# Optimization experiments

Hardware: AMD Instinct MI355X
Metric: run time of the kernel (lower is better)

Reference implementation:

```python
import jax, jax.numpy as jnp
import numpy as np

B, S, C, D, V, T = 64, 200, 32, 256, 10000, 1000


def _gru(x, Wih, Whh, bih, bhh):
    # x: [B,S,D]; PyTorch GRU, gate order (r, z, n)
    xp = jnp.einsum('bsd,gd->bsg', x, Wih) + bih  # [B,S,3D] input projections precomputed

    def step(h, xt):
        hp = h @ Whh.T + bhh
        xr, xz, xn = jnp.split(xt, 3, axis=-1)
        hr, hz, hn = jnp.split(hp, 3, axis=-1)
        r = jax.nn.sigmoid(xr + hr)
        z = jax.nn.sigmoid(xz + hz)
        n = jnp.tanh(xn + r * hn)
        h = (1.0 - z) * n + z * h
        return h, h

    h0 = jnp.zeros((x.shape[0], Whh.shape[1]), x.dtype)
    _, hs = jax.lax.scan(step, h0, jnp.swapaxes(xp, 0, 1))
    return jnp.swapaxes(hs, 0, 1)


def _pool(rnn, wl_W, wl_b, out_W, out_b):
    w = jnp.einsum('bsd,od->bso', rnn, wl_W) + wl_b      # [B,S,1]
    att = jax.nn.softmax(w[..., 0], axis=1)               # softmax over seq
    feat = jnp.sum(rnn * att[:, :, None], axis=1)         # [B,D]
    return feat @ out_W.T + out_b                          # [B,2]


def setup_inputs() -> dict:
    key = jax.random.key(0)
    ks = jax.random.split(key, 24)

    def n(i, shape, s=0.05):
        return jax.random.normal(ks[i], shape, dtype=jnp.float32) * s

    inp = {}
    inp['input_seqs'] = jax.random.randint(ks[0], (B, S, C), 0, V)
    inp['masks'] = jnp.ones((B, S), jnp.float32)
    inp['lengths'] = jax.random.randint(ks[1], (B,), 1, S)
    inp['seq_time_step'] = jax.random.uniform(ks[2], (B, S), dtype=jnp.float32)
    inp['code_masks'] = jnp.ones((B, S, C), jnp.float32)
    inp['diffusion_t'] = jax.random.randint(ks[3], (B,), 0, T)
    # parameters
    inp['emb_table'] = n(4, (V + 1, D)).at[V].set(0.0)  # padding_idx row zeroed
    inp['gru_Wih'] = n(5, (3 * D, D))
    inp['gru_Whh'] = n(6, (3 * D, D))
    inp['gru_bih'] = n(7, (3 * D,))
    inp['gru_bhh'] = n(8, (3 * D,))
    inp['whk_W'] = n(9, (D, D))
    inp['whk_b'] = n(10, (D,))
    inp['w1_W'] = n(11, (64, 2 * D))
    inp['w1_b'] = n(12, (64,))
    inp['w2_W'] = n(13, (2, 64))
    inp['w2_b'] = n(14, (2,))
    inp['wl_W'] = n(15, (1, D))
    inp['wl_b'] = n(16, (1,))
    inp['out_W'] = n(17, (2, D))
    inp['out_b'] = n(18, (2,))
    inp['betas'] = jnp.linspace(1e-4, 2e-2, T).astype(jnp.float32)  # linear beta schedule
    inp['W_diff'] = n(19, (S, S))      # surrogate for UNet denoiser (see notes)
    inp['time_scale'] = n(20, (T,), 1.0)
    inp['normal_noise'] = jax.random.normal(ks[21], (B, S, D), dtype=jnp.float32)
    return inp


def reference(input_seqs, masks, lengths, seq_time_step, code_masks, diffusion_t,
              emb_table, gru_Wih, gru_Whh, gru_bih, gru_bhh,
              whk_W, whk_b, w1_W, w1_b, w2_W, w2_b, wl_W, wl_b, out_W, out_b,
              betas, W_diff, time_scale, normal_noise):
    # embedding sum over codes per visit (dropout is identity at eval)
    x = jnp.take(emb_table, input_seqs, axis=0).sum(axis=2)  # [B,S,D]
    rnn = _gru(x, gru_Wih, gru_Whh, gru_bih, gru_bhh)

    # per-timestep attention-gated blend. In the original, e_k is ALWAYS x[:,0:1]
    # and each step depends only on precomputed rnn[:, i-1], so the sequential
    # Python loop vectorizes exactly over the time axis.
    e_k = x[:, 0:1, :]                                              # [B,1,D]
    w_prev = jnp.einsum('bsd,ed->bse', rnn[:, :-1, :], whk_W) + whk_b  # [B,S-1,D]
    cat = jnp.concatenate([jnp.broadcast_to(e_k, w_prev.shape), w_prev], axis=-1)
    h = jnp.tanh(jnp.einsum('bse,fe->bsf', cat, w1_W) + w1_b)
    attn = jax.nn.softmax(jnp.einsum('bsf,gf->bsg', h, w2_W) + w2_b, axis=-1)  # [B,S-1,2]
    blended = e_k * attn[..., 0:1] + w_prev * attn[..., 1:2]
    aligned = jnp.concatenate([x[:, 0:1, :], blended], axis=1)      # [B,S,D]

    # diffusion forward noising
    alpha = jnp.cumprod(1.0 - betas)[diffusion_t][:, None, None]    # [B,1,1]
    x_noisy = aligned * jnp.sqrt(alpha) + normal_noise * jnp.sqrt(1.0 - alpha)
    # surrogate denoiser over channel(=seq) axis, timestep-conditioned
    predicted_noise = jnp.einsum('cs,bsd->bcd', W_diff, x_noisy) * time_scale[diffusion_t][:, None, None]

    gen_x = aligned + (normal_noise - predicted_noise)
    gen_rnn = _gru(gen_x, gru_Wih, gru_Whh, gru_bih, gru_bhh)

    pred = _pool(rnn, wl_W, wl_b, out_W, out_b)
    gen_pred = _pool(gen_rnn, wl_W, wl_b, out_W, out_b)
    return pred, gen_pred, predicted_noise, normal_noise
```

## Files before the change

kernel.cpp:

```cpp
#include <hip/hip_runtime.h>
#include <math.h>

constexpr int Bn = 64, Sn = 200, Cn = 32, Dn = 256, Vn = 10000, Tn = 1000;
constexpr int G3 = 3 * Dn;
constexpr int KP = 224;

typedef __fp16 h2_t __attribute__((ext_vector_type(2)));
typedef short bf16x8 __attribute__((ext_vector_type(8)));
typedef float f32x4 __attribute__((ext_vector_type(4)));

static __device__ __forceinline__ h2_t as_h2(uint v) {
  union { uint u; h2_t h; } c; c.u = v; return c.h;
}
static __device__ __forceinline__ uint as_u32(h2_t h) {
  union { h2_t h; uint u; } c; c.h = h; return c.u;
}
static __device__ __forceinline__ ushort f2bf(float f) {
  uint u = __float_as_uint(f);
  u += 0x7FFFu + ((u >> 16) & 1u);
  return (ushort)(u >> 16);
}

__global__ __launch_bounds__(256) void k_w2f16(const float* __restrict__ w,
    uint* __restrict__ o, int npairs) {
  int i = blockIdx.x * 256 + threadIdx.x;
  if (i < npairs) {
    h2_t pk = __builtin_amdgcn_cvt_pkrtz(w[2 * i], w[2 * i + 1]);
    o[i] = as_u32(pk);
  }
}

__global__ __launch_bounds__(256) void k_w2bf(const float* __restrict__ w,
    ushort* __restrict__ o, int n) {
  int i = blockIdx.x * 256 + threadIdx.x;
  if (i < n) o[i] = f2bf(w[i]);
}

__global__ __launch_bounds__(256) void k_wd2bf(const float* __restrict__ w,
    ushort* __restrict__ o) {
  int i = blockIdx.x * 256 + threadIdx.x;
  if (i < Sn * KP) {
    int r = i / KP, c = i % KP;
    o[i] = (c < Sn) ? f2bf(w[r * Sn + c]) : (ushort)0;
  }
}

__global__ __launch_bounds__(256) void k_embed_sum(const int* __restrict__ seqs,
    const float* __restrict__ emb, float* __restrict__ x, ushort* __restrict__ xbf) {
  const int bs = blockIdx.x;
  const int d = threadIdx.x;
  const int* row = seqs + (size_t)bs * Cn;
  float acc = 0.f;
#pragma unroll
  for (int c = 0; c < Cn; ++c) acc += emb[(size_t)row[c] * Dn + d];
  x[(size_t)bs * Dn + d] = acc;
  xbf[(size_t)bs * Dn + d] = f2bf(acc);
}

__global__ __launch_bounds__(256) void k_gemm_bf16(const ushort* __restrict__ A,
    const ushort* __restrict__ Bm, const float* __restrict__ bias,
    float* __restrict__ C, int M, int N) {
  __shared__ ushort As[64 * 40];
  __shared__ ushort Bs[64 * 40];
  const int tid = threadIdx.x;
  const int m0 = blockIdx.x * 64, n0 = blockIdx.y * 64;
  const int wave = tid >> 6, lane = tid & 63;
  const int wr = wave >> 1, wc = wave & 1;
  const int lrow = tid >> 2, lseg = (tid & 3) * 8;
  const int r16 = lane & 15, kg = lane >> 4;
  f32x4 acc[2][2] = {};
  for (int k0 = 0; k0 < 256; k0 += 32) {
    *(uint4*)&As[lrow * 40 + lseg] =
        *(const uint4*)&A[(size_t)(m0 + lrow) * 256 + k0 + lseg];
    *(uint4*)&Bs[lrow * 40 + lseg] =
        *(const uint4*)&Bm[(size_t)(n0 + lrow) * 256 + k0 + lseg];
    __syncthreads();
    bf16x8 a0 = *(const bf16x8*)&As[(wr * 32 + r16) * 40 + kg * 8];
    bf16x8 a1 = *(const bf16x8*)&As[(wr * 32 + 16 + r16) * 40 + kg * 8];
    bf16x8 b0 = *(const bf16x8*)&Bs[(wc * 32 + r16) * 40 + kg * 8];
    bf16x8 b1 = *(const bf16x8*)&Bs[(wc * 32 + 16 + r16) * 40 + kg * 8];
    acc[0][0] = __builtin_amdgcn_mfma_f32_16x16x32_bf16(a0, b0, acc[0][0], 0, 0, 0);
    acc[0][1] = __builtin_amdgcn_mfma_f32_16x16x32_bf16(a0, b1, acc[0][1], 0, 0, 0);
    acc[1][0] = __builtin_amdgcn_mfma_f32_16x16x32_bf16(a1, b0, acc[1][0], 0, 0, 0);
    acc[1][1] = __builtin_amdgcn_mfma_f32_16x16x32_bf16(a1, b1, acc[1][1], 0, 0, 0);
    __syncthreads();
  }
#pragma unroll
  for (int mi = 0; mi < 2; ++mi)
#pragma unroll
    for (int ni = 0; ni < 2; ++ni)
#pragma unroll
      for (int r = 0; r < 4; ++r) {
        int gr = m0 + wr * 32 + mi * 16 + kg * 4 + r;
        int gc = n0 + wc * 32 + ni * 16 + r16;
        C[(size_t)gr * N + gc] = acc[mi][ni][r] + bias[gc];
      }
}

__global__ __launch_bounds__(768, 3) void k_gru_g(const float* __restrict__ xp,
    const uint* __restrict__ Wh, const float* __restrict__ bhh,
    float* __restrict__ out, ushort* __restrict__ out_bf) {
  const int b = blockIdx.x;
  const int tid = threadIdx.x;
  const int g = tid >> 8;
  const int d = tid & 255;
  __shared__ uint h2s[2][128];
  __shared__ float red[768];

  uint w_[128];
#pragma unroll
  for (int i = 0; i < 128; i += 4) {
    uint4 v = *reinterpret_cast<const uint4*>(Wh + (size_t)(g * 256 + d) * 128 + i);
    w_[i] = v.x; w_[i + 1] = v.y; w_[i + 2] = v.z; w_[i + 3] = v.w;
  }
  const float* xpb = xp + (size_t)b * Sn * G3;
  const float bias = bhh[g * 256 + d];
  float xv = (g == 2) ? 0.f : xpb[g * 256 + d];
  float xnv = (g == 0) ? xpb[512 + d] : 0.f;
  float h_old = 0.f;
  if (tid < 128) h2s[0][tid] = 0u;
  __syncthreads();

  for (int t = 0; t < Sn; ++t) {
    const int cur = t & 1;
    float a0 = 0.f, a1 = 0.f;
#pragma unroll
    for (int c = 0; c < 8; ++c) {
      uint4 v0 = *reinterpret_cast<const uint4*>(&h2s[cur][8 * c]);
      uint4 v1 = *reinterpret_cast<const uint4*>(&h2s[cur][8 * c + 4]);
      uint hh[8] = {v0.x, v0.y, v0.z, v0.w, v1.x, v1.y, v1.z, v1.w};
#pragma unroll
      for (int i = 0; i < 8; ++i)
        a0 = __builtin_amdgcn_fdot2(as_h2(w_[8 * c + i]), as_h2(hh[i]), a0, false);
    }
#pragma unroll
    for (int c = 8; c < 16; ++c) {
      uint4 v0 = *reinterpret_cast<const uint4*>(&h2s[cur][8 * c]);
      uint4 v1 = *reinterpret_cast<const uint4*>(&h2s[cur][8 * c + 4]);
      uint hh[8] = {v0.x, v0.y, v0.z, v0.w, v1.x, v1.y, v1.z, v1.w};
#pragma unroll
      for (int i = 0; i < 8; ++i)
        a1 = __builtin_amdgcn_fdot2(as_h2(w_[8 * c + i]), as_h2(hh[i]), a1, false);
    }
    red[tid] = a0 + a1 + xv + bias;
    float xnv_c = xnv;
    if (t + 1 < Sn) {
      const float* xr = xpb + (size_t)(t + 1) * G3;
      if (g != 2) xv = xr[g * 256 + d];
      if (g == 0) xnv = xr[512 + d];
    }
    __syncthreads();
    if (g == 0) {
      float rv = 1.f / (1.f + __expf(-red[d]));
      float zv = 1.f / (1.f + __expf(-red[256 + d]));
      float nv = tanhf(xnv_c + rv * red[512 + d]);
      float h = (1.f - zv) * nv + zv * h_old;
      h_old = h;
      const size_t oi = ((size_t)b * Sn + t) * Dn + d;
      out[oi] = h;
      if (out_bf) out_bf[oi] = f2bf(h);
      float hp2 = __shfl_xor(h, 1);
      if ((d & 1) == 0) h2s[cur ^ 1][d >> 1] = as_u32(__builtin_amdgcn_cvt_pkrtz(h, hp2));
    }
    __syncthreads();
  }
}

__global__ __launch_bounds__(256) void k_attn_par(const float* __restrict__ x,
    const float* __restrict__ wprev, const float* __restrict__ w1W,
    const float* __restrict__ w1b, const float* __restrict__ w2W,
    const float* __restrict__ w2b, float* __restrict__ aligned) {
  extern __shared__ float sm[];
  float* w1s = sm;
  float* ek  = w1s + 64 * 513;
  float* wp  = ek + 256;
  float* eks = wp + 256;
  float* t1  = eks + 64;
  float* a01 = t1 + 64;
  const int b = blockIdx.x, cy = blockIdx.y, tid = threadIdx.x;
  for (int idx = tid; idx < 64 * 512; idx += 256) {
    int f = idx >> 9, c = idx & 511;
    w1s[f * 513 + c] = w1W[idx];
  }
  ek[tid] = x[(size_t)b * Sn * Dn + tid];
  __syncthreads();
  const int f = tid >> 2, kq = tid & 3;
  {
    float p = 0.f;
    const float* wr = w1s + f * 513;
#pragma unroll 8
    for (int j = 0; j < 64; ++j) {
      int k = 64 * kq + ((j + 16 * kq) & 63);
      p += ek[k] * wr[k];
    }
    p += __shfl_xor(p, 1);
    p += __shfl_xor(p, 2);
    if (kq == 0) eks[f] = p + w1b[f];
  }
  if (cy == 0) aligned[(size_t)b * Sn * Dn + tid] = ek[tid];
  __syncthreads();
  const int s0 = 1 + cy * 29;
  const int s1 = (s0 + 29 < Sn) ? s0 + 29 : Sn;
  for (int s = s0; s < s1; ++s) {
    wp[tid] = wprev[((size_t)b * Sn + (s - 1)) * Dn + tid];
    __syncthreads();
    float p = 0.f;
    const float* wr = w1s + f * 513 + 256;
#pragma unroll 8
    for (int j = 0; j < 64; ++j) {
      int k = 64 * kq + ((j + 16 * kq) & 63);
      p += wp[k] * wr[k];
    }
    p += __shfl_xor(p, 1);
    p += __shfl_xor(p, 2);
    if (kq == 0) t1[f] = tanhf(eks[f] + p);
    __syncthreads();
    if (tid == 0) {
      float l0 = w2b[0], l1 = w2b[1];
#pragma unroll
      for (int j = 0; j < 64; ++j) { l0 += t1[j] * w2W[j]; l1 += t1[j] * w2W[64 + j]; }
      float m = fmaxf(l0, l1);
      float e0 = __expf(l0 - m), e1 = __expf(l1 - m);
      float inv = 1.f / (e0 + e1);
      a01[0] = e0 * inv; a01[1] = e1 * inv;
    }
    __syncthreads();
    aligned[((size_t)b * Sn + s) * Dn + tid] = ek[tid] * a01[0] + wp[tid] * a01[1];
    __syncthreads();
  }
}

__global__ __launch_bounds__(256) void k_cumsetup(const float* __restrict__ betas,
    const int* __restrict__ difft, const float* __restrict__ tscale,
    float* __restrict__ sa, float* __restrict__ sb, float* __restrict__ tsv) {
  __shared__ float bl[Tn];
  const int tid = threadIdx.x;
  for (int i = tid; i < Tn; i += 256) bl[i] = betas[i];
  __syncthreads();
  if (tid == 0) {
    float p = 1.f;
    for (int t = 0; t < Tn; ++t) { p *= (1.f - bl[t]); bl[t] = p; }
  }
  __syncthreads();
  if (tid < Bn) {
    int tb = difft[tid];
    float a = bl[tb];
    sa[tid] = sqrtf(a);
    sb[tid] = sqrtf(1.f - a);
    tsv[tid] = tscale[tb];
  }
}

__global__ __launch_bounds__(256) void k_noisy_t(const float* __restrict__ aligned,
    const float* __restrict__ noise, const float* __restrict__ sa,
    const float* __restrict__ sb, ushort* __restrict__ xnT) {
  __shared__ float T[256][33];
  const int b = blockIdx.x, sy = blockIdx.y;
  const int tid = threadIdx.x;
  const float A = sa[b], Bc = sb[b];
#pragma unroll 4
  for (int i = 0; i < 32; ++i) {
    int s = 32 * sy + i;
    float v = 0.f;
    if (s < Sn) {
      size_t idx = ((size_t)b * Sn + s) * Dn + tid;
      v = aligned[idx] * A + noise[idx] * Bc;
    }
    T[tid][i] = v;
  }
  __syncthreads();
  const int sl = tid & 31, dq = tid >> 5;
#pragma unroll 4
  for (int dd = 0; dd < 32; ++dd) {
    int d = dq * 32 + dd;
    xnT[((size_t)b * Dn + d) * KP + 32 * sy + sl] = f2bf(T[d][sl]);
  }
}

__global__ __launch_bounds__(256) void k_diff_mfma(const ushort* __restrict__ Wd_bf,
    const ushort* __restrict__ xnT, const float* __restrict__ tsv,
    const float* __restrict__ aligned, const float* __restrict__ noise,
    float* __restrict__ pn, ushort* __restrict__ genx_bf) {
  __shared__ ushort As[64 * 40];
  __shared__ ushort Bs[64 * 40];
  const int bz = blockIdx.z;
  const int tid = threadIdx.x;
  const int m0 = blockIdx.x * 64, n0 = blockIdx.y * 64;
  const int wave = tid >> 6, lane = tid & 63;
  const int wr = wave >> 1, wc = wave & 1;
  const int lrow = tid >> 2, lseg = (tid & 3) * 8;
  const int r16 = lane & 15, kg = lane >> 4;
  const ushort* Bb = xnT + (size_t)bz * Dn * KP;
  f32x4 acc[2][2] = {};
  for (int k0 = 0; k0 < KP; k0 += 32) {
    uint4 av = {0u, 0u, 0u, 0u};
    if (m0 + lrow < Sn)
      av = *(const uint4*)&Wd_bf[(size_t)(m0 + lrow) * KP + k0 + lseg];
    *(uint4*)&As[lrow * 40 + lseg] = av;
    *(uint4*)&Bs[lrow * 40 + lseg] =
        *(const uint4*)&Bb[(size_t)(n0 + lrow) * KP + k0 + lseg];
    __syncthreads();
    bf16x8 a0 = *(const bf16x8*)&As[(wr * 32 + r16) * 40 + kg * 8];
    bf16x8 a1 = *(const bf16x8*)&As[(wr * 32 + 16 + r16) * 40 + kg * 8];
    bf16x8 b0 = *(const bf16x8*)&Bs[(wc * 32 + r16) * 40 + kg * 8];
    bf16x8 b1 = *(const bf16x8*)&Bs[(wc * 32 + 16 + r16) * 40 + kg * 8];
    acc[0][0] = __builtin_amdgcn_mfma_f32_16x16x32_bf16(a0, b0, acc[0][0], 0, 0, 0);
    acc[0][1] = __builtin_amdgcn_mfma_f32_16x16x32_bf16(a0, b1, acc[0][1], 0, 0, 0);
    acc[1][0] = __builtin_amdgcn_mfma_f32_16x16x32_bf16(a1, b0, acc[1][0], 0, 0, 0);
    acc[1][1] = __builtin_amdgcn_mfma_f32_16x16x32_bf16(a1, b1, acc[1][1], 0, 0, 0);
    __syncthreads();
  }
  const float ts = tsv[bz];
#pragma unroll
  for (int mi = 0; mi < 2; ++mi)
#pragma unroll
    for (int ni = 0; ni < 2; ++ni)
#pragma unroll
      for (int r = 0; r < 4; ++r) {
        int gr = m0 + wr * 32 + mi * 16 + kg * 4 + r;
        int gc = n0 + wc * 32 + ni * 16 + r16;
        if (gr < Sn) {
          size_t idx = ((size_t)bz * Sn + gr) * Dn + gc;
          float val = acc[mi][ni][r] * ts;
          pn[idx] = val;
          genx_bf[idx] = f2bf(aligned[idx] + noise[idx] - val);
        }
      }
}

__global__ __launch_bounds__(256) void k_pool(const float* __restrict__ rnn,
    const float* __restrict__ wlW, const float* __restrict__ wlb,
    const float* __restrict__ outW, const float* __restrict__ outb,
    float* __restrict__ out2) {
  const int b = blockIdx.x, tid = threadIdx.x;
  __shared__ float wl[Dn], att[256], red[256], feat[Dn];
  wl[tid] = wlW[tid];
  __syncthreads();
  float wv = -1e30f;
  if (tid < Sn) {
    const float* r = rnn + ((size_t)b * Sn + tid) * Dn;
    float a = wlb[0];
    for (int k = 0; k < Dn; ++k) a += r[k] * wl[k];
    wv = a;
  }
  red[tid] = wv;
  __syncthreads();
  for (int off = 128; off > 0; off >>= 1) {
    if (tid < off) red[tid] = fmaxf(red[tid], red[tid + off]);
    __syncthreads();
  }
  const float m = red[0];
  __syncthreads();
  float e = (tid < Sn) ? __expf(wv - m) : 0.f;
  red[tid] = e;
  __syncthreads();
  for (int off = 128; off > 0; off >>= 1) {
    if (tid < off) red[tid] += red[tid + off];
    __syncthreads();
  }
  const float inv = 1.f / red[0];
  att[tid] = e * inv;
  __syncthreads();
  const float* rb = rnn + (size_t)b * Sn * Dn;
  float a = 0.f;
  for (int s = 0; s < Sn; ++s) a += rb[(size_t)s * Dn + tid] * att[s];
  feat[tid] = a;
  __syncthreads();
  if (tid < 2) {
    float acc = outb[tid];
    for (int k = 0; k < Dn; ++k) acc += feat[k] * outW[tid * Dn + k];
    out2[b * 2 + tid] = acc;
  }
}

extern "C" void kernel_launch(void* const* d_in, const int* in_sizes, int n_in,
                              void* d_out, int out_size, void* d_ws, size_t ws_size,
                              hipStream_t stream) {
  const int*   seqs   = (const int*)  d_in[0];
  const int*   difft  = (const int*)  d_in[5];
  const float* emb    = (const float*)d_in[6];
  const float* Wih    = (const float*)d_in[7];
  const float* Whh    = (const float*)d_in[8];
  const float* bih    = (const float*)d_in[9];
  const float* bhh    = (const float*)d_in[10];
  const float* whkW   = (const float*)d_in[11];
  const float* whkb   = (const float*)d_in[12];
  const float* w1W    = (const float*)d_in[13];
  const float* w1b    = (const float*)d_in[14];
  const float* w2W    = (const float*)d_in[15];
  const float* w2b    = (const float*)d_in[16];
  const float* wlW    = (const float*)d_in[17];
  const float* wlb    = (const float*)d_in[18];
  const float* outW   = (const float*)d_in[19];
  const float* outb   = (const float*)d_in[20];
  const float* betas  = (const float*)d_in[21];
  const float* Wd     = (const float*)d_in[22];
  const float* tscale = (const float*)d_in[23];
  const float* noise  = (const float*)d_in[24];

  float* ws = (float*)d_ws;
  const size_t NX  = (size_t)Bn * Sn * Dn;
  const size_t NXP = (size_t)Bn * Sn * G3;
  float* x       = ws;
  float* xp      = ws + NX;
  ushort* xnT    = (ushort*)xp;
  float* aligned = xp + NX;
  float* rnn     = ws + NX + NXP;
  float* wprev   = ws + 2 * NX + NXP;
  ushort* x_bf   = (ushort*)wprev;
  ushort* genx_bf= (ushort*)wprev;
  float* sa      = ws + 3 * NX + NXP;
  float* sb      = sa + 64;
  float* tsv     = sb + 64;
  uint*  Wf16    = (uint*)(tsv + 64);
  ushort* rnn_bf = (ushort*)(Wf16 + 98304);
  ushort* Wih_bf = rnn_bf + NX;
  ushort* whk_bf = Wih_bf + 196608;
  ushort* Wd_bf  = whk_bf + 65536;

  float* out       = (float*)d_out;
  float* pred      = out;
  float* gpred     = out + 128;
  float* pn        = out + 256;
  float* out_noise = out + 256 + NX;

  const int ATTN_SMEM = (64 * 513 + 256 + 256 + 64 + 64 + 2) * 4;

  k_w2f16<<<dim3(384), dim3(256), 0, stream>>>(Whh, Wf16, 98304);
  k_w2bf<<<dim3(768), dim3(256), 0, stream>>>(Wih, Wih_bf, 196608);
  k_w2bf<<<dim3(256), dim3(256), 0, stream>>>(whkW, whk_bf, 65536);
  k_wd2bf<<<dim3(175), dim3(256), 0, stream>>>(Wd, Wd_bf);
  k_embed_sum<<<dim3(Bn * Sn), dim3(Dn), 0, stream>>>(seqs, emb, x, x_bf);
  k_gemm_bf16<<<dim3(200, 12), dim3(256), 0, stream>>>(x_bf, Wih_bf, bih, xp, Bn * Sn, G3);
  k_gru_g<<<dim3(Bn), dim3(768), 0, stream>>>(xp, Wf16, bhh, rnn, rnn_bf);
  k_gemm_bf16<<<dim3(200, 4), dim3(256), 0, stream>>>(rnn_bf, whk_bf, whkb, wprev, Bn * Sn, Dn);
  k_attn_par<<<dim3(Bn, 7), dim3(256), ATTN_SMEM, stream>>>(x, wprev, w1W, w1b, w2W, w2b, aligned);
  k_cumsetup<<<dim3(1), dim3(256), 0, stream>>>(betas, difft, tscale, sa, sb, tsv);
  k_noisy_t<<<dim3(Bn, 7), dim3(256), 0, stream>>>(aligned, noise, sa, sb, xnT);
  k_diff_mfma<<<dim3(4, 4, Bn), dim3(256), 0, stream>>>(Wd_bf, xnT, tsv, aligned, noise, pn, genx_bf);
  k_gemm_bf16<<<dim3(200, 12), dim3(256), 0, stream>>>(genx_bf, Wih_bf, bih, xp, Bn * Sn, G3);
  k_gru_g<<<dim3(Bn), dim3(768), 0, stream>>>(xp, Wf16, bhh, wprev, (ushort*)nullptr);
  k_pool<<<dim3(Bn), dim3(256), 0, stream>>>(rnn, wlW, wlb, outW, outb, pred);
  k_pool<<<dim3(Bn), dim3(256), 0, stream>>>(wprev, wlW, wlb, outW, outb, gpred);
  (void)hipMemcpyAsync(out_noise, noise, NX * sizeof(float), hipMemcpyDeviceToDevice, stream);
}
```

Baseline: 1.018 ms.

## Restructure GRU matvec thread mapping with swizzled weights and bf16-only outputs

The GRU recurrent kernel now has each group of 4 threads split the K dimension of 4 gate rows. Weights are pre-permuted with a bank-conflict-avoiding swizzle, so each thread reads one 16-byte LDS chunk per j and reuses it across 4 rows, with shuffles combining partial sums. This targets LDS traffic and bank conflicts on the serial recurrence path. The GRU also stops writing fp32 hidden states, and the pooling kernels read the bf16 copies instead, cutting memory traffic at some precision cost. The attention softmax logit reduction moves from a single-thread loop to a wavefront shuffle reduction.

```diff
diff --git a/kernel.cpp b/kernel.cpp
--- a/kernel.cpp
+++ b/kernel.cpp
@@ -20,14 +20,23 @@
   u += 0x7FFFu + ((u >> 16) & 1u);
   return (ushort)(u >> 16);
 }
-
-__global__ __launch_bounds__(256) void k_w2f16(const float* __restrict__ w,
-    uint* __restrict__ o, int npairs) {
-  int i = blockIdx.x * 256 + threadIdx.x;
-  if (i < npairs) {
-    h2_t pk = __builtin_amdgcn_cvt_pkrtz(w[2 * i], w[2 * i + 1]);
-    o[i] = as_u32(pk);
-  }
+static __device__ __forceinline__ float bf2f(ushort b) {
+  return __uint_as_float((uint)b << 16);
+}
+
+__global__ __launch_bounds__(256) void k_wprep(const float* __restrict__ w,
+    uint* __restrict__ o) {
+  int idx = blockIdx.x * 256 + threadIdx.x;
+  if (idx >= 768 * 128) return;
+  int t = idx >> 7, rem = idx & 127;
+  int m = rem >> 5, j = (rem >> 2) & 7, ii = rem & 3;
+  int q = t & 3, r = t >> 2;
+  int c = 8 * q + ((j + 2 * q) & 7);
+  int row = r + 192 * m;
+  int pairidx = 4 * c + ii;
+  h2_t pk = __builtin_amdgcn_cvt_pkrtz(w[(size_t)row * Dn + 2 * pairidx],
+                                       w[(size_t)row * Dn + 2 * pairidx + 1]);
+  o[idx] = as_u32(pk);
 }
 
 __global__ __launch_bounds__(256) void k_w2bf(const float* __restrict__ w,
@@ -97,70 +106,87 @@
       }
 }
 
-__global__ __launch_bounds__(768, 3) void k_gru_g(const float* __restrict__ xp,
-    const uint* __restrict__ Wh, const float* __restrict__ bhh,
-    float* __restrict__ out, ushort* __restrict__ out_bf) {
+__global__ __launch_bounds__(768, 3) void k_gru_c(const float* __restrict__ xp,
+    const uint* __restrict__ Wq, const float* __restrict__ bhh,
+    ushort* __restrict__ out_bf) {
   const int b = blockIdx.x;
   const int tid = threadIdx.x;
-  const int g = tid >> 8;
-  const int d = tid & 255;
+  const int q = tid & 3;
+  const int r = tid >> 2;
   __shared__ uint h2s[2][128];
   __shared__ float red[768];
 
   uint w_[128];
-#pragma unroll
-  for (int i = 0; i < 128; i += 4) {
-    uint4 v = *reinterpret_cast<const uint4*>(Wh + (size_t)(g * 256 + d) * 128 + i);
-    w_[i] = v.x; w_[i + 1] = v.y; w_[i + 2] = v.z; w_[i + 3] = v.w;
+  {
+    const uint* src = Wq + (size_t)tid * 128;
+#pragma unroll
+    for (int i = 0; i < 128; i += 4) {
+      uint4 v = *reinterpret_cast<const uint4*>(src + i);
+      w_[i] = v.x; w_[i + 1] = v.y; w_[i + 2] = v.z; w_[i + 3] = v.w;
+    }
   }
   const float* xpb = xp + (size_t)b * Sn * G3;
-  const float bias = bhh[g * 256 + d];
-  float xv = (g == 2) ? 0.f : xpb[g * 256 + d];
-  float xnv = (g == 0) ? xpb[512 + d] : 0.f;
+  float bias_[4], xv_[4];
+#pragma unroll
+  for (int m = 0; m < 4; ++m) {
+    int row = r + 192 * m;
+    bias_[m] = bhh[row];
+    xv_[m] = (row < 512) ? xpb[row] : 0.f;
+  }
+  float xnv = (tid < 256) ? xpb[512 + tid] : 0.f;
   float h_old = 0.f;
   if (tid < 128) h2s[0][tid] = 0u;
   __syncthreads();
 
+  int caddr[8];
+#pragma unroll
+  for (int j = 0; j < 8; ++j) caddr[j] = 4 * (8 * q + ((j + 2 * q) & 7));
+
   for (int t = 0; t < Sn; ++t) {
     const int cur = t & 1;
-    float a0 = 0.f, a1 = 0.f;
-#pragma unroll
-    for (int c = 0; c < 8; ++c) {
-      uint4 v0 = *reinterpret_cast<const uint4*>(&h2s[cur][8 * c]);
-      uint4 v1 = *reinterpret_cast<const uint4*>(&h2s[cur][8 * c + 4]);
-      uint hh[8] = {v0.x, v0.y, v0.z, v0.w, v1.x, v1.y, v1.z, v1.w};
-#pragma unroll
-      for (int i = 0; i < 8; ++i)
-        a0 = __builtin_amdgcn_fdot2(as_h2(w_[8 * c + i]), as_h2(hh[i]), a0, false);
-    }
-#pragma unroll
-    for (int c = 8; c < 16; ++c) {
-      uint4 v0 = *reinterpret_cast<const uint4*>(&h2s[cur][8 * c]);
-      uint4 v1 = *reinterpret_cast<const uint4*>(&h2s[cur][8 * c + 4]);
-      uint hh[8] = {v0.x, v0.y, v0.z, v0.w, v1.x, v1.y, v1.z, v1.w};
-#pragma unroll
-      for (int i = 0; i < 8; ++i)
-        a1 = __builtin_amdgcn_fdot2(as_h2(w_[8 * c + i]), as_h2(hh[i]), a1, false);
-    }
-    red[tid] = a0 + a1 + xv + bias;
+    const uint* base = &h2s[cur][0];
+    float acc0 = 0.f, acc1 = 0.f, acc2 = 0.f, acc3 = 0.f;
+#pragma unroll
+    for (int j = 0; j < 8; ++j) {
+      uint4 hv = *reinterpret_cast<const uint4*>(base + caddr[j]);
+      uint hh[4] = {hv.x, hv.y, hv.z, hv.w};
+#pragma unroll
+      for (int ii = 0; ii < 4; ++ii) {
+        h2_t hx = as_h2(hh[ii]);
+        acc0 = __builtin_amdgcn_fdot2(as_h2(w_[(0 * 8 + j) * 4 + ii]), hx, acc0, false);
+        acc1 = __builtin_amdgcn_fdot2(as_h2(w_[(1 * 8 + j) * 4 + ii]), hx, acc1, false);
+        acc2 = __builtin_amdgcn_fdot2(as_h2(w_[(2 * 8 + j) * 4 + ii]), hx, acc2, false);
+        acc3 = __builtin_amdgcn_fdot2(as_h2(w_[(3 * 8 + j) * 4 + ii]), hx, acc3, false);
+      }
+    }
+    float a_[4] = {acc0, acc1, acc2, acc3};
+#pragma unroll
+    for (int m = 0; m < 4; ++m) {
+      float v = a_[m];
+      v += __shfl_xor(v, 1);
+      v += __shfl_xor(v, 2);
+      if (q == 0) red[r + 192 * m] = v + xv_[m] + bias_[m];
+    }
     float xnv_c = xnv;
     if (t + 1 < Sn) {
       const float* xr = xpb + (size_t)(t + 1) * G3;
-      if (g != 2) xv = xr[g * 256 + d];
-      if (g == 0) xnv = xr[512 + d];
-    }
-    __syncthreads();
-    if (g == 0) {
-      float rv = 1.f / (1.f + __expf(-red[d]));
-      float zv = 1.f / (1.f + __expf(-red[256 + d]));
-      float nv = tanhf(xnv_c + rv * red[512 + d]);
+#pragma unroll
+      for (int m = 0; m < 4; ++m) {
+        int row = r + 192 * m;
+        if (row < 512) xv_[m] = xr[row];
+      }
+      if (tid < 256) xnv = xr[512 + tid];
+    }
+    __syncthreads();
+    if (tid < 256) {
+      float rv = 1.f / (1.f + __expf(-red[tid]));
+      float zv = 1.f / (1.f + __expf(-red[256 + tid]));
+      float nv = tanhf(xnv_c + rv * red[512 + tid]);
       float h = (1.f - zv) * nv + zv * h_old;
       h_old = h;
-      const size_t oi = ((size_t)b * Sn + t) * Dn + d;
-      out[oi] = h;
-      if (out_bf) out_bf[oi] = f2bf(h);
+      out_bf[((size_t)b * Sn + t) * Dn + tid] = f2bf(h);
       float hp2 = __shfl_xor(h, 1);
-      if ((d & 1) == 0) h2s[cur ^ 1][d >> 1] = as_u32(__builtin_amdgcn_cvt_pkrtz(h, hp2));
+      if ((tid & 1) == 0) h2s[cur ^ 1][tid >> 1] = as_u32(__builtin_amdgcn_cvt_pkrtz(h, hp2));
     }
     __syncthreads();
   }
@@ -183,6 +209,9 @@
     w1s[f * 513 + c] = w1W[idx];
   }
   ek[tid] = x[(size_t)b * Sn * Dn + tid];
+  const float w2a = (tid < 64) ? w2W[tid] : 0.f;
+  const float w2c = (tid < 64) ? w2W[64 + tid] : 0.f;
+  const float wb0 = w2b[0], wb1 = w2b[1];
   __syncthreads();
   const int f = tid >> 2, kq = tid & 3;
   {
@@ -215,14 +244,21 @@
     p += __shfl_xor(p, 2);
     if (kq == 0) t1[f] = tanhf(eks[f] + p);
     __syncthreads();
-    if (tid == 0) {
-      float l0 = w2b[0], l1 = w2b[1];
-#pragma unroll
-      for (int j = 0; j < 64; ++j) { l0 += t1[j] * w2W[j]; l1 += t1[j] * w2W[64 + j]; }
-      float m = fmaxf(l0, l1);
-      float e0 = __expf(l0 - m), e1 = __expf(l1 - m);
-      float inv = 1.f / (e0 + e1);
-      a01[0] = e0 * inv; a01[1] = e1 * inv;
+    if (tid < 64) {
+      float tv = t1[tid];
+      float v0 = tv * w2a, v1 = tv * w2c;
+#pragma unroll
+      for (int off = 32; off > 0; off >>= 1) {
+        v0 += __shfl_xor(v0, off);
+        v1 += __shfl_xor(v1, off);
+      }
+      if (tid == 0) {
+        float l0 = v0 + wb0, l1 = v1 + wb1;
+        float m = fmaxf(l0, l1);
+        float e0 = __expf(l0 - m), e1 = __expf(l1 - m);
+        float inv = 1.f / (e0 + e1);
+        a01[0] = e0 * inv; a01[1] = e1 * inv;
+      }
     }
     __syncthreads();
     aligned[((size_t)b * Sn + s) * Dn + tid] = ek[tid] * a01[0] + wp[tid] * a01[1];
@@ -328,7 +364,7 @@
       }
 }
 
-__global__ __launch_bounds__(256) void k_pool(const float* __restrict__ rnn,
+__global__ __launch_bounds__(256) void k_pool_bf(const ushort* __restrict__ rnn,
     const float* __restrict__ wlW, const float* __restrict__ wlb,
     const float* __restrict__ outW, const float* __restrict__ outb,
     float* __restrict__ out2) {
@@ -338,9 +374,18 @@
   __syncthreads();
   float wv = -1e30f;
   if (tid < Sn) {
-    const float* r = rnn + ((size_t)b * Sn + tid) * Dn;
+    const ushort* rp = rnn + ((size_t)b * Sn + tid) * Dn;
     float a = wlb[0];
-    for (int k = 0; k < Dn; ++k) a += r[k] * wl[k];
+#pragma unroll 4
+    for (int k0 = 0; k0 < Dn; k0 += 8) {
+      uint4 v = *reinterpret_cast<const uint4*>(rp + k0);
+      uint vv[4] = {v.x, v.y, v.z, v.w};
+#pragma unroll
+      for (int i = 0; i < 4; ++i) {
+        a += bf2f((ushort)(vv[i] & 0xFFFF)) * wl[k0 + 2 * i];
+        a += bf2f((ushort)(vv[i] >> 16)) * wl[k0 + 2 * i + 1];
+      }
+    }
     wv = a;
   }
   red[tid] = wv;
@@ -361,9 +406,9 @@
   const float inv = 1.f / red[0];
   att[tid] = e * inv;
   __syncthreads();
-  const float* rb = rnn + (size_t)b * Sn * Dn;
+  const ushort* rb = rnn + (size_t)b * Sn * Dn;
   float a = 0.f;
-  for (int s = 0; s < Sn; ++s) a += rb[(size_t)s * Dn + tid] * att[s];
+  for (int s = 0; s < Sn; ++s) a += bf2f(rb[(size_t)s * Dn + tid]) * att[s];
   feat[tid] = a;
   __syncthreads();
   if (tid < 2) {
@@ -405,15 +450,15 @@
   float* xp      = ws + NX;
   ushort* xnT    = (ushort*)xp;
   float* aligned = xp + NX;
-  float* rnn     = ws + NX + NXP;
-  float* wprev   = ws + 2 * NX + NXP;
+  float* wprev   = ws + NX + NXP;
   ushort* x_bf   = (ushort*)wprev;
   ushort* genx_bf= (ushort*)wprev;
-  float* sa      = ws + 3 * NX + NXP;
+  ushort* gen_bf = ((ushort*)wprev) + NX;
+  float* sa      = ws + 2 * NX + NXP;
   float* sb      = sa + 64;
   float* tsv     = sb + 64;
-  uint*  Wf16    = (uint*)(tsv + 64);
-  ushort* rnn_bf = (ushort*)(Wf16 + 98304);
+  uint*  Wq      = (uint*)(tsv + 64);
+  ushort* rnn_bf = (ushort*)(Wq + 98304);
   ushort* Wih_bf = rnn_bf + NX;
   ushort* whk_bf = Wih_bf + 196608;
   ushort* Wd_bf  = whk_bf + 65536;
@@ -426,21 +471,21 @@
 
   const int ATTN_SMEM = (64 * 513 + 256 + 256 + 64 + 64 + 2) * 4;
 
-  k_w2f16<<<dim3(384), dim3(256), 0, stream>>>(Whh, Wf16, 98304);
+  k_wprep<<<dim3(384), dim3(256), 0, stream>>>(Whh, Wq);
   k_w2bf<<<dim3(768), dim3(256), 0, stream>>>(Wih, Wih_bf, 196608);
   k_w2bf<<<dim3(256), dim3(256), 0, stream>>>(whkW, whk_bf, 65536);
   k_wd2bf<<<dim3(175), dim3(256), 0, stream>>>(Wd, Wd_bf);
   k_embed_sum<<<dim3(Bn * Sn), dim3(Dn), 0, stream>>>(seqs, emb, x, x_bf);
   k_gemm_bf16<<<dim3(200, 12), dim3(256), 0, stream>>>(x_bf, Wih_bf, bih, xp, Bn * Sn, G3);
-  k_gru_g<<<dim3(Bn), dim3(768), 0, stream>>>(xp, Wf16, bhh, rnn, rnn_bf);
+  k_gru_c<<<dim3(Bn), dim3(768), 0, stream>>>(xp, Wq, bhh, rnn_bf);
   k_gemm_bf16<<<dim3(200, 4), dim3(256), 0, stream>>>(rnn_bf, whk_bf, whkb, wprev, Bn * Sn, Dn);
   k_attn_par<<<dim3(Bn, 7), dim3(256), ATTN_SMEM, stream>>>(x, wprev, w1W, w1b, w2W, w2b, aligned);
   k_cumsetup<<<dim3(1), dim3(256), 0, stream>>>(betas, difft, tscale, sa, sb, tsv);
   k_noisy_t<<<dim3(Bn, 7), dim3(256), 0, stream>>>(aligned, noise, sa, sb, xnT);
   k_diff_mfma<<<dim3(4, 4, Bn), dim3(256), 0, stream>>>(Wd_bf, xnT, tsv, aligned, noise, pn, genx_bf);
   k_gemm_bf16<<<dim3(200, 12), dim3(256), 0, stream>>>(genx_bf, Wih_bf, bih, xp, Bn * Sn, G3);
-  k_gru_g<<<dim3(Bn), dim3(768), 0, stream>>>(xp, Wf16, bhh, wprev, (ushort*)nullptr);
-  k_pool<<<dim3(Bn), dim3(256), 0, stream>>>(rnn, wlW, wlb, outW, outb, pred);
-  k_pool<<<dim3(Bn), dim3(256), 0, stream>>>(wprev, wlW, wlb, outW, outb, gpred);
+  k_gru_c<<<dim3(Bn), dim3(768), 0, stream>>>(xp, Wq, bhh, gen_bf);
+  k_pool_bf<<<dim3(Bn), dim3(256), 0, stream>>>(rnn_bf, wlW, wlb, outW, outb, pred);
+  k_pool_bf<<<dim3(Bn), dim3(256), 0, stream>>>(gen_bf, wlW, wlb, outW, outb, gpred);
   (void)hipMemcpyAsync(out_noise, noise, NX * sizeof(float), hipMemcpyDeviceToDevice, stream);
 }
```

Result: slower. 1.834 ms (+80.1%).
